# Kernel tuning notes

Hardware: AMD Instinct MI355X
Metric: run time of the kernel (lower is better)

## Reference

```python
import jax, jax.numpy as jnp
import numpy as np
from functools import partial

EPS = 1e-10


@partial(jax.custom_vjp, nondiff_argnums=(1,))
def kwta(x, k):
    # k-WTA: keep top-k values along last dim, zero elsewhere (STE backward).
    vals, _ = jax.lax.top_k(x, k)
    thresh = vals[..., -1:]
    return jnp.where(x >= thresh, x, jnp.zeros((), x.dtype))


def _kwta_fwd(x, k):
    out = kwta(x, k)
    mask = (out != 0).astype(x.dtype)  # matches torch: mask = (out != 0)
    return out, mask


def _kwta_bwd(k, mask, g):
    return (g * mask,)


kwta.defvjp(_kwta_fwd, _kwta_bwd)


def _sparsify(x, W_down, k):
    h = jax.nn.relu(x @ W_down.T)          # (B, T, N_ca3)
    h = kwta(h, k)
    norm = jnp.maximum(jnp.linalg.norm(h, axis=-1, keepdims=True), EPS)
    return h / norm


def _retrieve_successor(sparse, W_ca3, k):
    # retrieval_steps = 1; replicate the early-break on all-zero activity.
    h = jax.nn.relu(sparse @ W_ca3.T)       # (B, T, N_ca3)
    valid = h.sum() >= EPS
    hk = kwta(h, k)
    norm = jnp.maximum(jnp.linalg.norm(hk, axis=-1, keepdims=True), EPS)
    return jnp.where(valid, hk / norm, sparse)


def setup_inputs() -> dict:
    key = jax.random.key(0)
    k1, k2, k3, k4, k5, k6 = jax.random.split(key, 6)
    B, T, D, N = 4, 2048, 1024, 4096
    x = jax.random.normal(k1, (B, T, D), dtype=jnp.float32)
    # xavier_normal: std = gain * sqrt(2 / (fan_in + fan_out))
    W_down = jax.random.normal(k2, (N, D), dtype=jnp.float32) * (0.5 * np.sqrt(2.0 / (D + N)))
    W_up = jax.random.normal(k3, (D, N), dtype=jnp.float32) * (0.1 * np.sqrt(2.0 / (D + N)))
    # gate_proj weight is zero-init in torch; use small random for a nontrivial gate
    W_gate = jax.random.normal(k4, (D, D), dtype=jnp.float32) * 0.02
    b_gate = jnp.full((D,), -2.0, dtype=jnp.float32)
    # W_ca3 buffer is zero-init then Hebbian-learned; random stand-in
    W_ca3 = jax.random.normal(k6, (N, N), dtype=jnp.float32) * 0.02
    return {"x": x, "W_down": W_down, "W_up": W_up, "W_gate": W_gate,
            "b_gate": b_gate, "W_ca3": W_ca3, "k": 64}


def reference(x, W_down, W_up, W_gate, b_gate, W_ca3, k):
    sparse = _sparsify(x, W_down, k)                    # (B, T, N)
    successor = _retrieve_successor(sparse, W_ca3, k)   # (B, T, N)
    prediction = successor @ W_up.T                     # (B, T, D)
    g = jax.nn.sigmoid(x @ W_gate.T + b_gate)           # (B, T, D)
    return x + g * prediction
```

## Files before the change

### kernel.cpp

```cpp
#include <hip/hip_runtime.h>
#include <hip/hip_bf16.h>
#include <stdint.h>

typedef float f32x4 __attribute__((ext_vector_type(4)));
typedef int i32x4 __attribute__((ext_vector_type(4)));

#define MROWS 8192
#define DD 1024
#define DN 4096

__device__ __forceinline__ void load_lds16(const void* g, void* l) {
  __builtin_amdgcn_global_load_lds((const __attribute__((address_space(1))) void*)g,
                                   (__attribute__((address_space(3))) void*)l, 16, 0, 0);
}

__device__ __forceinline__ unsigned f32_to_bf16_rne(float f) {
  unsigned u = __float_as_uint(f);
  return (u + 0x7fffu + ((u >> 16) & 1u)) >> 16;
}

template<int EPI>
__global__ void __launch_bounds__(512, 1)
gemm_i8_4ph(const uint8_t* __restrict__ A, const uint8_t* __restrict__ B,
            __hip_bfloat16* __restrict__ Cb, int M, int N, int K,
            float* __restrict__ vsum,
            const float* __restrict__ sA, const float* __restrict__ sB)
{
  extern __shared__ __align__(16) char smem[];
  const int tid  = threadIdx.x;
  const int lane = tid & 63;
  const int wave = tid >> 6;
  const int wm = wave >> 2;
  const int wn = wave & 3;

  const int nwg = gridDim.x;
  const int bid = ((int)blockIdx.x % 8) * (nwg >> 3) + ((int)blockIdx.x >> 3);

  const int nbn = N >> 8;
  const int bm = (bid / nbn) << 8;
  const int bn = (bid % nbn) << 8;

  const int NT = K >> 7;

  i32x4 acc[8][4];
  const i32x4 izero = {0, 0, 0, 0};
#pragma unroll
  for (int i = 0; i < 8; ++i)
#pragma unroll
    for (int j = 0; j < 4; ++j)
      acc[i][j] = izero;

  const int csb = (((tid & 3) ^ ((tid >> 3) & 3)) << 4);
  const uint8_t* Ag = A + (size_t)(bm + (tid >> 2)) * K + csb;
  const uint8_t* Bg = B + (size_t)(bn + (tid >> 2)) * K + csb;

  const int rl = lane & 15;
  const int kc = lane >> 4;
  const int chunk_off = ((kc ^ ((rl >> 1) & 3)) << 4);
  const int aoff = ((wm << 7) + rl) * 64 + chunk_off;
  const int boff = ((wn << 6) + rl) * 64 + chunk_off;

#define STAGE_AB(S, KH) do { \
    const int kt_ = (((S) & (NT - 1)) << 7) + ((KH) << 6); \
    char* da_ = smem + (((((S) & 1) << 1) | (KH)) << 14) + (tid << 4); \
    load_lds16(Ag + kt_, da_); \
    load_lds16(Ag + (size_t)128 * K + kt_, da_ + 8192); \
    load_lds16(Bg + kt_, da_ + 65536); \
    load_lds16(Bg + (size_t)128 * K + kt_, da_ + 65536 + 8192); \
  } while (0)

  i32x4 a0, a1, a2, a3, a4, a5, a6, a7, b0, b1, b2, b3;

#define MFMA_ROW8(MI, AF) \
    acc[MI][0] = __builtin_amdgcn_mfma_i32_16x16x64_i8(AF, b0, acc[MI][0], 0, 0, 0); \
    acc[MI][1] = __builtin_amdgcn_mfma_i32_16x16x64_i8(AF, b1, acc[MI][1], 0, 0, 0); \
    acc[MI][2] = __builtin_amdgcn_mfma_i32_16x16x64_i8(AF, b2, acc[MI][2], 0, 0, 0); \
    acc[MI][3] = __builtin_amdgcn_mfma_i32_16x16x64_i8(AF, b3, acc[MI][3], 0, 0, 0);

#define PH4(P, KH, STG) do { \
    { const char* ab_ = smem + ((((P) << 1) | (KH)) << 14) + aoff; \
      a0 = *(const i32x4*)(ab_);        a1 = *(const i32x4*)(ab_ + 1024); \
      a2 = *(const i32x4*)(ab_ + 2048); a3 = *(const i32x4*)(ab_ + 3072); \
      a4 = *(const i32x4*)(ab_ + 4096); a5 = *(const i32x4*)(ab_ + 5120); \
      a6 = *(const i32x4*)(ab_ + 6144); a7 = *(const i32x4*)(ab_ + 7168); \
      const char* bb_ = smem + 65536 + ((((P) << 1) | (KH)) << 14) + boff; \
      b0 = *(const i32x4*)(bb_);        b1 = *(const i32x4*)(bb_ + 1024); \
      b2 = *(const i32x4*)(bb_ + 2048); b3 = *(const i32x4*)(bb_ + 3072); } \
    STG; \
    asm volatile("s_waitcnt vmcnt(8)" ::: "memory"); \
    asm volatile("s_barrier" ::: "memory"); \
    asm volatile("s_waitcnt lgkmcnt(0)" ::: "memory"); \
    __builtin_amdgcn_sched_barrier(0); \
    __builtin_amdgcn_s_setprio(1); \
    MFMA_ROW8(0, a0) MFMA_ROW8(1, a1) MFMA_ROW8(2, a2) MFMA_ROW8(3, a3) \
    MFMA_ROW8(4, a4) MFMA_ROW8(5, a5) MFMA_ROW8(6, a6) MFMA_ROW8(7, a7) \
    __builtin_amdgcn_s_setprio(0); \
    asm volatile("s_barrier" ::: "memory"); \
  } while (0)

  STAGE_AB(0, 0);
  STAGE_AB(0, 1);
  STAGE_AB(1, 0);
  asm volatile("s_waitcnt vmcnt(8)" ::: "memory");
  asm volatile("s_barrier" ::: "memory");

#pragma unroll 1
  for (int t = 0; t < NT; t += 2) {
    PH4(0, 0, STAGE_AB(t + 1, 1));
    PH4(0, 1, STAGE_AB(t + 2, 0));
    PH4(1, 0, STAGE_AB(t + 2, 1));
    PH4(1, 1, STAGE_AB(t + 3, 0));
  }

  const int r0 = bm + (wm << 7) + (kc << 2);
  const int c0 = bn + (wn << 6) + rl;
  float lsum = 0.f;
#pragma unroll
  for (int mi = 0; mi < 8; ++mi) {
#pragma unroll
    for (int nf = 0; nf < 4; ++nf) {
#pragma unroll
      for (int q = 0; q < 4; ++q) {
        const int r = r0 + (mi << 4) + q;
        const int c = c0 + (nf << 4);
        float v = (float)acc[mi][nf][q] * sA[r] * sB[c];
        v = fmaxf(v, 0.f);
        Cb[(size_t)r * N + c] = __float2bfloat16(v);
        if constexpr (EPI == 1) lsum += v;
      }
    }
  }
  if constexpr (EPI == 1) {
#pragma unroll
    for (int off = 32; off > 0; off >>= 1)
      lsum += __shfl_down(lsum, off);
    if (lane == 0) atomicAdd(vsum, lsum);
  }

#undef STAGE_AB
#undef MFMA_ROW8
#undef PH4
}

__global__ void __launch_bounds__(256)
gemm_predgate(const uint8_t* __restrict__ Asp, const uint8_t* __restrict__ Bup,
              const uint8_t* __restrict__ Ax,  const uint8_t* __restrict__ Bg8,
              float* __restrict__ Cf, int M, int N, int K1, int K2,
              const float* __restrict__ sA,  const float* __restrict__ swu,
              const float* __restrict__ sx,  const float* __restrict__ swg,
              const float* __restrict__ Xf,  const float* __restrict__ Bgate)
{
  __shared__ __align__(16) char smem[32768];
  const int tid  = threadIdx.x;
  const int lane = tid & 63;
  const int wave = tid >> 6;

  const int nbn = N >> 7;
  const int bm = ((int)blockIdx.x / nbn) << 7;
  const int bn = ((int)blockIdx.x % nbn) << 7;

  const int wm = (wave >> 1) << 6;
  const int wn = (wave & 1) << 6;

  i32x4 acc1[4][4], acc2[4][4];
  const i32x4 izero = {0, 0, 0, 0};
#pragma unroll
  for (int i = 0; i < 4; ++i)
#pragma unroll
    for (int j = 0; j < 4; ++j) { acc1[i][j] = izero; acc2[i][j] = izero; }

  const int srow = tid >> 3;
  const int schk = (tid & 7) ^ (srow & 7);
  char* ldsA = smem + (wave << 10);
  char* ldsB = smem + 16384 + (wave << 10);

  const int aoff0 = (wm + (lane & 15)) << 7;
  const int boff0 = 16384 + ((wn + (lane & 15)) << 7);
  const int kc = lane >> 4;
  const int sw = lane & 7;

#define K_LOOP(APTR, BPTR, KK, ACC) do { \
    const uint8_t* Ag = (APTR) + (size_t)(bm + srow) * (KK) + (schk << 4); \
    const uint8_t* Bg = (BPTR) + (size_t)(bn + srow) * (KK) + (schk << 4); \
    for (int k0 = 0; k0 < (KK); k0 += 128) { \
      _Pragma("unroll") \
      for (int i = 0; i < 4; ++i) \
        load_lds16(Ag + (size_t)(i << 5) * (KK) + k0, ldsA + (i << 12)); \
      _Pragma("unroll") \
      for (int i = 0; i < 4; ++i) \
        load_lds16(Bg + (size_t)(i << 5) * (KK) + k0, ldsB + (i << 12)); \
      __syncthreads(); \
      _Pragma("unroll") \
      for (int ks = 0; ks < 2; ++ks) { \
        const int cb = ((kc + (ks << 2)) ^ sw) << 4; \
        i32x4 af[4], bfr[4]; \
        _Pragma("unroll") \
        for (int i = 0; i < 4; ++i) \
          af[i] = *reinterpret_cast<const i32x4*>(smem + aoff0 + (i << 11) + cb); \
        _Pragma("unroll") \
        for (int j = 0; j < 4; ++j) \
          bfr[j] = *reinterpret_cast<const i32x4*>(smem + boff0 + (j << 11) + cb); \
        _Pragma("unroll") \
        for (int i = 0; i < 4; ++i) \
          _Pragma("unroll") \
          for (int j = 0; j < 4; ++j) \
            ACC[i][j] = __builtin_amdgcn_mfma_i32_16x16x64_i8(af[i], bfr[j], ACC[i][j], 0, 0, 0); \
      } \
      __syncthreads(); \
    } \
  } while (0)

  K_LOOP(Asp, Bup, K1, acc1);
  K_LOOP(Ax,  Bg8, K2, acc2);
#undef K_LOOP

  const int r0 = bm + wm + ((lane >> 4) << 2);
  const int c0 = bn + wn + (lane & 15);
#pragma unroll
  for (int i = 0; i < 4; ++i) {
#pragma unroll
    for (int j = 0; j < 4; ++j) {
#pragma unroll
      for (int q = 0; q < 4; ++q) {
        const int r = r0 + (i << 4) + q;
        const int c = c0 + (j << 4);
        const size_t idx = (size_t)r * N + c;
        const float pred = (float)acc1[i][j][q] * sA[r] * swu[c];
        const float vg   = (float)acc2[i][j][q] * sx[r] * swg[c] + Bgate[c];
        const float g = 1.f / (1.f + __expf(-vg));
        Cf[idx] = Xf[idx] + g * pred;
      }
    }
  }
}

template<int MODE>
__global__ void __launch_bounds__(256)
kwta_wave(const __hip_bfloat16* __restrict__ H, uint8_t* __restrict__ OUTQ,
          float* __restrict__ sA, const float* __restrict__ vsumPtr,
          const int* __restrict__ kptr)
{
  const int tid  = threadIdx.x;
  const int lane = tid & 63;
  const int w    = tid >> 6;
  const int row  = ((int)blockIdx.x << 2) + w;

  if constexpr (MODE == 1) {
    if (!(*vsumPtr >= 1e-10f)) return;
  }

  const uint4* h8 = (const uint4*)(H + (size_t)row * 4096);
  uint4 d[8];
#pragma unroll
  for (int i = 0; i < 8; ++i) d[i] = h8[(i << 6) + lane];

  const unsigned k = (unsigned)(*kptr);

  unsigned kmax = 0;
#pragma unroll
  for (int i = 0; i < 8; ++i) {
    const unsigned* p = (const unsigned*)&d[i];
#pragma unroll
    for (int c4 = 0; c4 < 4; ++c4) {
      kmax = max(kmax, p[c4] & 0xffffu);
      kmax = max(kmax, p[c4] >> 16);
    }
  }
#pragma unroll
  for (int off = 32; off > 0; off >>= 1) kmax = max(kmax, __shfl_xor(kmax, off));

  unsigned lo = 0, hi = 65536;
#pragma unroll 1
  for (int it = 0; it < 16; ++it) {
    const unsigned mid = (lo + hi) >> 1;
    unsigned c = 0;
#pragma unroll
    for (int i = 0; i < 8; ++i) {
      const unsigned* p = (const unsigned*)&d[i];
#pragma unroll
      for (int c4 = 0; c4 < 4; ++c4) {
        c += ((p[c4] & 0xffffu) >= mid) ? 1u : 0u;
        c += ((p[c4] >> 16) >= mid) ? 1u : 0u;
      }
    }
#pragma unroll
    for (int off = 32; off > 0; off >>= 1) c += __shfl_xor(c, off);
    if (c >= k) lo = mid; else hi = mid;
  }
  const unsigned threshKey = lo;

  float ss = 0.f;
#pragma unroll
  for (int i = 0; i < 8; ++i) {
    const unsigned* p = (const unsigned*)&d[i];
#pragma unroll
    for (int c4 = 0; c4 < 4; ++c4) {
#pragma unroll
      for (int hh = 0; hh < 2; ++hh) {
        const unsigned key = hh ? (p[c4] >> 16) : (p[c4] & 0xffffu);
        if (key >= threshKey) {
          const float v = __uint_as_float(key << 16);
          ss = fmaf(v, v, ss);
        }
      }
    }
  }
#pragma unroll
  for (int off = 32; off > 0; off >>= 1) ss += __shfl_xor(ss, off);
  const float inv = 1.f / fmaxf(sqrtf(ss), 1e-10f);

  const float vmaxf = __uint_as_float(kmax << 16);
  const float r127 = (kmax > 0) ? 127.f / vmaxf : 0.f;

  if (lane == 0) sA[row] = vmaxf * inv * (1.f / 127.f);

  uint2* o2 = (uint2*)(OUTQ + (size_t)row * 4096);
#pragma unroll
  for (int i = 0; i < 8; ++i) {
    const unsigned* p = (const unsigned*)&d[i];
    unsigned b[8];
#pragma unroll
    for (int c4 = 0; c4 < 4; ++c4) {
#pragma unroll
      for (int hh = 0; hh < 2; ++hh) {
        const unsigned key = hh ? (p[c4] >> 16) : (p[c4] & 0xffffu);
        unsigned q = 0;
        if (key >= threshKey && key > 0) {
          const float v = __uint_as_float(key << 16);
          q = (unsigned)__float2int_rn(v * r127) & 0xffu;
        }
        b[c4 * 2 + hh] = q;
      }
    }
    uint2 o;
    o.x = b[0] | (b[1] << 8) | (b[2] << 16) | (b[3] << 24);
    o.y = b[4] | (b[5] << 8) | (b[6] << 16) | (b[7] << 24);
    o2[(i << 6) + lane] = o;
  }
}

__global__ void __launch_bounds__(256)
quant1024(const float* __restrict__ X, const float* __restrict__ Wd,
          const float* __restrict__ Wg,
          uint8_t* __restrict__ xq, uint8_t* __restrict__ wdq,
          uint8_t* __restrict__ wgq,
          float* __restrict__ sx, float* __restrict__ swd,
          float* __restrict__ swg)
{
  const int wgl = ((int)blockIdx.x << 2) + (threadIdx.x >> 6);
  const int lane = threadIdx.x & 63;

  const float* W; uint8_t* q; float* s; int row;
  if      (wgl < 8192)  { W = X;  q = xq;  s = sx;  row = wgl; }
  else if (wgl < 12288) { W = Wd; q = wdq; s = swd; row = wgl - 8192; }
  else                  { W = Wg; q = wgq; s = swg; row = wgl - 12288; }

  const float4* src = (const float4*)(W + (size_t)row * 1024);
  float4 v[4];
  float am = 0.f;
#pragma unroll
  for (int i = 0; i < 4; ++i) {
    v[i] = src[(i << 6) + lane];
    am = fmaxf(am, fmaxf(fmaxf(fabsf(v[i].x), fabsf(v[i].y)),
                         fmaxf(fabsf(v[i].z), fabsf(v[i].w))));
  }
#pragma unroll
  for (int off = 32; off > 0; off >>= 1) am = fmaxf(am, __shfl_xor(am, off));

  const float rinv = (am > 0.f) ? 127.f / am : 0.f;
  uint4 o;
  unsigned* ob = (unsigned*)&o;
#pragma unroll
  for (int i = 0; i < 4; ++i) {
    const unsigned b0 = (unsigned)__float2int_rn(v[i].x * rinv) & 0xffu;
    const unsigned b1 = (unsigned)__float2int_rn(v[i].y * rinv) & 0xffu;
    const unsigned b2 = (unsigned)__float2int_rn(v[i].z * rinv) & 0xffu;
    const unsigned b3 = (unsigned)__float2int_rn(v[i].w * rinv) & 0xffu;
    ob[i] = b0 | (b1 << 8) | (b2 << 16) | (b3 << 24);
  }
  ((uint4*)(q + (size_t)row * 1024))[lane] = o;
  if (lane == 0) s[row] = am * (1.f / 127.f);
}

__global__ void __launch_bounds__(256)
quant4096(const float* __restrict__ Wc, const float* __restrict__ Wu,
          uint8_t* __restrict__ qc, uint8_t* __restrict__ qu,
          float* __restrict__ sc, float* __restrict__ su)
{
  const int wgl = ((int)blockIdx.x << 2) + (threadIdx.x >> 6);
  const int lane = threadIdx.x & 63;

  const float* W; uint8_t* q; float* s; int row;
  if (wgl < 4096) { W = Wc; q = qc; s = sc; row = wgl; }
  else            { W = Wu; q = qu; s = su; row = wgl - 4096; }

  const float4* src = (const float4*)(W + (size_t)row * 4096);
  float4 v[16];
  float am = 0.f;
#pragma unroll
  for (int i = 0; i < 16; ++i) {
    v[i] = src[(i << 6) + lane];
    am = fmaxf(am, fmaxf(fmaxf(fabsf(v[i].x), fabsf(v[i].y)),
                         fmaxf(fabsf(v[i].z), fabsf(v[i].w))));
  }
#pragma unroll
  for (int off = 32; off > 0; off >>= 1) am = fmaxf(am, __shfl_xor(am, off));

  const float rinv = (am > 0.f) ? 127.f / am : 0.f;
  unsigned* qo = (unsigned*)(q + (size_t)row * 4096);
#pragma unroll
  for (int i = 0; i < 16; ++i) {
    const unsigned b0 = (unsigned)__float2int_rn(v[i].x * rinv) & 0xffu;
    const unsigned b1 = (unsigned)__float2int_rn(v[i].y * rinv) & 0xffu;
    const unsigned b2 = (unsigned)__float2int_rn(v[i].z * rinv) & 0xffu;
    const unsigned b3 = (unsigned)__float2int_rn(v[i].w * rinv) & 0xffu;
    qo[(i << 6) + lane] = b0 | (b1 << 8) | (b2 << 16) | (b3 << 24);
  }
  if (lane == 0) s[row] = am * (1.f / 127.f);
}

__global__ void diag_kernel(float* out, float mb)
{
  if (threadIdx.x == 0 && blockIdx.x == 0) out[0] = -mb;
}

extern "C" void kernel_launch(void* const* d_in, const int* in_sizes, int n_in,
                              void* d_out, int out_size, void* d_ws, size_t ws_size,
                              hipStream_t stream)
{
  const float* x     = (const float*)d_in[0];
  const float* Wdown = (const float*)d_in[1];
  const float* Wup   = (const float*)d_in[2];
  const float* Wgate = (const float*)d_in[3];
  const float* bgate = (const float*)d_in[4];
  const float* Wca3  = (const float*)d_in[5];
  const int*   kptr  = (const int*)d_in[6];

  const size_t OFF_XQ   = 0;
  const size_t OFF_WDQ  = 8388608;
  const size_t OFF_WGQ  = 12582912;
  const size_t OFF_WCQ  = 13631488;
  const size_t OFF_WUQ  = 30408704;
  const size_t OFF_SX   = 34603008;
  const size_t OFF_SWD  = 34635776;
  const size_t OFF_SWG  = 34652160;
  const size_t OFF_SWC  = 34656256;
  const size_t OFF_SWU  = 34672640;
  const size_t OFF_SA   = 34676736;
  const size_t OFF_VSUM = 34709504;
  const size_t OFF_SPQ  = 34713600;
  const size_t OFF_H    = 68268032;
  const size_t NEED     = 135376896;

  if (ws_size < NEED) {
    diag_kernel<<<1, 64, 0, stream>>>((float*)d_out, (float)(ws_size >> 20));
    return;
  }

  char* ws = (char*)d_ws;
  uint8_t*        xq   = (uint8_t*)       (ws + OFF_XQ);
  uint8_t*        wdq  = (uint8_t*)       (ws + OFF_WDQ);
  uint8_t*        wgq  = (uint8_t*)       (ws + OFF_WGQ);
  uint8_t*        wcq  = (uint8_t*)       (ws + OFF_WCQ);
  uint8_t*        wuq  = (uint8_t*)       (ws + OFF_WUQ);
  float*          sx   = (float*)         (ws + OFF_SX);
  float*          swd  = (float*)         (ws + OFF_SWD);
  float*          swg  = (float*)         (ws + OFF_SWG);
  float*          swc  = (float*)         (ws + OFF_SWC);
  float*          swu  = (float*)         (ws + OFF_SWU);
  float*          sA   = (float*)         (ws + OFF_SA);
  float*          vsum = (float*)         (ws + OFF_VSUM);
  uint8_t*        spq  = (uint8_t*)       (ws + OFF_SPQ);
  __hip_bfloat16* h    = (__hip_bfloat16*)(ws + OFF_H);

  hipMemsetAsync(vsum, 0, sizeof(float), stream);

  quant1024<<<3328, 256, 0, stream>>>(x, Wdown, Wgate, xq, wdq, wgq, sx, swd, swg);
  quant4096<<<1280, 256, 0, stream>>>(Wca3, Wup, wcq, wuq, swc, swu);

  gemm_i8_4ph<0><<<(MROWS >> 8) * (DN >> 8), 512, 131072, stream>>>(
      xq, wdq, h, MROWS, DN, DD, nullptr, sx, swd);
  kwta_wave<0><<<MROWS / 4, 256, 0, stream>>>(h, spq, sA, nullptr, kptr);
  gemm_i8_4ph<1><<<(MROWS >> 8) * (DN >> 8), 512, 131072, stream>>>(
      spq, wcq, h, MROWS, DN, DN, vsum, sA, swc);
  kwta_wave<1><<<MROWS / 4, 256, 0, stream>>>(h, spq, sA, vsum, kptr);
  gemm_predgate<<<(MROWS >> 7) * (DD >> 7), 256, 0, stream>>>(
      spq, wuq, xq, wgq, (float*)d_out, MROWS, DD, DN, DD,
      sA, swu, sx, swg, x, bgate);
}
```

Before: 465.0 us.

## Split int8 GEMM main loop into eight phases with register double-buffered A fragments

Restructures the main loop of the int8 MFMA GEMM from four phases to eight. Each phase computes half the M rows while prefetching the next A fragment set from LDS into a second register buffer, and issues the A and B global-to-LDS staging separately. The lgkmcnt(0) wait before the MFMAs is removed so LDS reads overlap matrix math, and the vmcnt thresholds are retuned. This trades more barriers per K step and higher register pressure for less exposed LDS latency, and the intricate phase parameters risk reading stale data.

After: 457.5 us. About the same (-1.6%).

```diff
diff --git a/kernel.cpp b/kernel.cpp
--- a/kernel.cpp
+++ b/kernel.cpp
@@ -14,14 +14,9 @@
                                    (__attribute__((address_space(3))) void*)l, 16, 0, 0);
 }
 
-__device__ __forceinline__ unsigned f32_to_bf16_rne(float f) {
-  unsigned u = __float_as_uint(f);
-  return (u + 0x7fffu + ((u >> 16) & 1u)) >> 16;
-}
-
 template<int EPI>
 __global__ void __launch_bounds__(512, 1)
-gemm_i8_4ph(const uint8_t* __restrict__ A, const uint8_t* __restrict__ B,
+gemm_i8_8ph(const uint8_t* __restrict__ A, const uint8_t* __restrict__ B,
             __hip_bfloat16* __restrict__ Cb, int M, int N, int K,
             float* __restrict__ vsum,
             const float* __restrict__ sA, const float* __restrict__ sB)
@@ -60,16 +55,22 @@
   const int aoff = ((wm << 7) + rl) * 64 + chunk_off;
   const int boff = ((wn << 6) + rl) * 64 + chunk_off;
 
-#define STAGE_AB(S, KH) do { \
+#define STAGE_A8(S, KH) do { \
     const int kt_ = (((S) & (NT - 1)) << 7) + ((KH) << 6); \
-    char* da_ = smem + (((((S) & 1) << 1) | (KH)) << 14) + (tid << 4); \
-    load_lds16(Ag + kt_, da_); \
-    load_lds16(Ag + (size_t)128 * K + kt_, da_ + 8192); \
-    load_lds16(Bg + kt_, da_ + 65536); \
-    load_lds16(Bg + (size_t)128 * K + kt_, da_ + 65536 + 8192); \
+    char* dst_ = smem + (((((S) & 1) << 1) | (KH)) << 14) + (tid << 4); \
+    load_lds16(Ag + kt_, dst_); \
+    load_lds16(Ag + (size_t)128 * K + kt_, dst_ + 8192); \
   } while (0)
 
-  i32x4 a0, a1, a2, a3, a4, a5, a6, a7, b0, b1, b2, b3;
+#define STAGE_B8(S, KH) do { \
+    const int kt_ = (((S) & (NT - 1)) << 7) + ((KH) << 6); \
+    char* dst_ = smem + 65536 + (((((S) & 1) << 1) | (KH)) << 14) + (tid << 4); \
+    load_lds16(Bg + kt_, dst_); \
+    load_lds16(Bg + (size_t)128 * K + kt_, dst_ + 8192); \
+  } while (0)
+
+  i32x4 afS[2][4];
+  i32x4 b0, b1, b2, b3;
 
 #define MFMA_ROW8(MI, AF) \
     acc[MI][0] = __builtin_amdgcn_mfma_i32_16x16x64_i8(AF, b0, acc[MI][0], 0, 0, 0); \
@@ -77,39 +78,55 @@
     acc[MI][2] = __builtin_amdgcn_mfma_i32_16x16x64_i8(AF, b2, acc[MI][2], 0, 0, 0); \
     acc[MI][3] = __builtin_amdgcn_mfma_i32_16x16x64_i8(AF, b3, acc[MI][3], 0, 0, 0);
 
-#define PH4(P, KH, STG) do { \
-    { const char* ab_ = smem + ((((P) << 1) | (KH)) << 14) + aoff; \
-      a0 = *(const i32x4*)(ab_);        a1 = *(const i32x4*)(ab_ + 1024); \
-      a2 = *(const i32x4*)(ab_ + 2048); a3 = *(const i32x4*)(ab_ + 3072); \
-      a4 = *(const i32x4*)(ab_ + 4096); a5 = *(const i32x4*)(ab_ + 5120); \
-      a6 = *(const i32x4*)(ab_ + 6144); a7 = *(const i32x4*)(ab_ + 7168); \
-      const char* bb_ = smem + 65536 + ((((P) << 1) | (KH)) << 14) + boff; \
-      b0 = *(const i32x4*)(bb_);        b1 = *(const i32x4*)(bb_ + 1024); \
-      b2 = *(const i32x4*)(bb_ + 2048); b3 = *(const i32x4*)(bb_ + 3072); } \
+#define PH8(PN, KHN, MHN, ASETN, ACUR, MHC, DOBP, BP, BKH, STG, VM) do { \
+    { const char* ab_ = smem + ((((PN) << 1) | (KHN)) << 14) + aoff + (MHN) * 4096; \
+      afS[ASETN][0] = *(const i32x4*)(ab_); \
+      afS[ASETN][1] = *(const i32x4*)(ab_ + 1024); \
+      afS[ASETN][2] = *(const i32x4*)(ab_ + 2048); \
+      afS[ASETN][3] = *(const i32x4*)(ab_ + 3072); } \
     STG; \
-    asm volatile("s_waitcnt vmcnt(8)" ::: "memory"); \
+    if (VM) { asm volatile("s_waitcnt vmcnt(6)" ::: "memory"); } \
     asm volatile("s_barrier" ::: "memory"); \
-    asm volatile("s_waitcnt lgkmcnt(0)" ::: "memory"); \
     __builtin_amdgcn_sched_barrier(0); \
     __builtin_amdgcn_s_setprio(1); \
-    MFMA_ROW8(0, a0) MFMA_ROW8(1, a1) MFMA_ROW8(2, a2) MFMA_ROW8(3, a3) \
-    MFMA_ROW8(4, a4) MFMA_ROW8(5, a5) MFMA_ROW8(6, a6) MFMA_ROW8(7, a7) \
+    MFMA_ROW8((MHC) * 4 + 0, afS[ACUR][0]) \
+    MFMA_ROW8((MHC) * 4 + 1, afS[ACUR][1]) \
+    MFMA_ROW8((MHC) * 4 + 2, afS[ACUR][2]) \
+    MFMA_ROW8((MHC) * 4 + 3, afS[ACUR][3]) \
     __builtin_amdgcn_s_setprio(0); \
+    if (DOBP) { \
+      const char* bb_ = smem + 65536 + ((((BP) << 1) | (BKH)) << 14) + boff; \
+      b0 = *(const i32x4*)(bb_); b1 = *(const i32x4*)(bb_ + 1024); \
+      b2 = *(const i32x4*)(bb_ + 2048); b3 = *(const i32x4*)(bb_ + 3072); } \
     asm volatile("s_barrier" ::: "memory"); \
   } while (0)
 
-  STAGE_AB(0, 0);
-  STAGE_AB(0, 1);
-  STAGE_AB(1, 0);
-  asm volatile("s_waitcnt vmcnt(8)" ::: "memory");
+  STAGE_A8(0, 0); STAGE_B8(0, 0);
+  STAGE_A8(0, 1); STAGE_B8(0, 1);
+  STAGE_A8(1, 0); STAGE_B8(1, 0);
+  asm volatile("s_waitcnt vmcnt(4)" ::: "memory");
   asm volatile("s_barrier" ::: "memory");
+  {
+    const char* ab_ = smem + aoff;
+    afS[1][0] = *(const i32x4*)(ab_);
+    afS[1][1] = *(const i32x4*)(ab_ + 1024);
+    afS[1][2] = *(const i32x4*)(ab_ + 2048);
+    afS[1][3] = *(const i32x4*)(ab_ + 3072);
+    const char* bb_ = smem + 65536 + boff;
+    b0 = *(const i32x4*)(bb_); b1 = *(const i32x4*)(bb_ + 1024);
+    b2 = *(const i32x4*)(bb_ + 2048); b3 = *(const i32x4*)(bb_ + 3072);
+  }
 
 #pragma unroll 1
   for (int t = 0; t < NT; t += 2) {
-    PH4(0, 0, STAGE_AB(t + 1, 1));
-    PH4(0, 1, STAGE_AB(t + 2, 0));
-    PH4(1, 0, STAGE_AB(t + 2, 1));
-    PH4(1, 1, STAGE_AB(t + 3, 0));
+    PH8(0, 0, 1, 0, 1, 0, 0, 0, 0, STAGE_A8(t + 1, 1), 1);
+    PH8(0, 1, 0, 1, 0, 1, 1, 0, 1, STAGE_B8(t + 1, 1), 0);
+    PH8(0, 1, 1, 0, 1, 0, 0, 0, 0, STAGE_A8(t + 2, 0), 1);
+    PH8(1, 0, 0, 1, 0, 1, 1, 1, 0, STAGE_B8(t + 2, 0), 0);
+    PH8(1, 0, 1, 0, 1, 0, 0, 0, 0, STAGE_A8(t + 2, 1), 1);
+    PH8(1, 1, 0, 1, 0, 1, 1, 1, 1, STAGE_B8(t + 2, 1), 0);
+    PH8(1, 1, 1, 0, 1, 0, 0, 0, 0, STAGE_A8(t + 3, 0), 1);
+    PH8(0, 0, 0, 1, 0, 1, 1, 0, 0, STAGE_B8(t + 3, 0), 0);
   }
 
   const int r0 = bm + (wm << 7) + (kc << 2);
@@ -137,9 +154,10 @@
     if (lane == 0) atomicAdd(vsum, lsum);
   }
 
-#undef STAGE_AB
+#undef STAGE_A8
+#undef STAGE_B8
 #undef MFMA_ROW8
-#undef PH4
+#undef PH8
 }
 
 __global__ void __launch_bounds__(256)
@@ -478,10 +496,10 @@
   quant1024<<<3328, 256, 0, stream>>>(x, Wdown, Wgate, xq, wdq, wgq, sx, swd, swg);
   quant4096<<<1280, 256, 0, stream>>>(Wca3, Wup, wcq, wuq, swc, swu);
 
-  gemm_i8_4ph<0><<<(MROWS >> 8) * (DN >> 8), 512, 131072, stream>>>(
+  gemm_i8_8ph<0><<<(MROWS >> 8) * (DN >> 8), 512, 131072, stream>>>(
       xq, wdq, h, MROWS, DN, DD, nullptr, sx, swd);
   kwta_wave<0><<<MROWS / 4, 256, 0, stream>>>(h, spq, sA, nullptr, kptr);
-  gemm_i8_4ph<1><<<(MROWS >> 8) * (DN >> 8), 512, 131072, stream>>>(
+  gemm_i8_8ph<1><<<(MROWS >> 8) * (DN >> 8), 512, 131072, stream>>>(
       spq, wcq, h, MROWS, DN, DN, vsum, sA, swc);
   kwta_wave<1><<<MROWS / 4, 256, 0, stream>>>(h, spq, sA, vsum, kptr);
   gemm_predgate<<<(MROWS >> 7) * (DD >> 7), 256, 0, stream>>>(
```
